# Performance work log

Hardware: AMD Instinct MI355X
Metric: run time of the kernel (lower is better)

Reference implementation:

```python
import jax, jax.numpy as jnp
import numpy as np
import math

B, S = 1, 2048
HID = 4096
NH = 32            # total query heads
NKV = 8            # total kv heads
D = HID // NH      # 128 head_dim
WIN = 1024         # sliding window (layer_idx=1 is odd and < num_layers//2)
LAYER = 1
THETA = 10000.0
LAMBDA_INIT = 0.8 - 0.6 * math.exp(-0.3 * LAYER)
SCALE = D ** -0.5
EPS = 1e-5
OP = NH * D + 2 * NKV * D  # Wqkv output size


def setup_inputs() -> dict:
    key = jax.random.key(0)
    ks = jax.random.split(key, 9)
    std = 0.02
    return {
        "hidden_states": jax.random.normal(ks[0], (B * S, HID), jnp.float32),
        "positions": jnp.tile(jnp.arange(S, dtype=jnp.int32), B),
        "Wqkv_w": jax.random.normal(ks[1], (OP, HID), jnp.float32) * std,
        "Wqkv_b": jnp.zeros((OP,), jnp.float32),
        "out_w": jax.random.normal(ks[2], (HID, NH * D), jnp.float32) * std,
        "out_b": jnp.zeros((HID,), jnp.float32),
        "lambda_q1": jax.random.normal(ks[3], (D,), jnp.float32) * 0.1,
        "lambda_k1": jax.random.normal(ks[4], (D,), jnp.float32) * 0.1,
        "lambda_q2": jax.random.normal(ks[5], (D,), jnp.float32) * 0.1,
        "lambda_k2": jax.random.normal(ks[6], (D,), jnp.float32) * 0.1,
        "subln_w": jnp.ones((2 * D,), jnp.float32),
    }


def _rope(x, pos):
    # neox-style rotary; x: [N, H, D], pos: [N]
    half = D // 2
    inv_freq = 1.0 / (THETA ** (jnp.arange(half, dtype=jnp.float32) / half))
    ang = pos.astype(jnp.float32)[:, None] * inv_freq[None, :]      # [N, half]
    cos = jnp.cos(ang)[:, None, :]
    sin = jnp.sin(ang)[:, None, :]
    x1, x2 = x[..., :half], x[..., half:]
    return jnp.concatenate([x1 * cos - x2 * sin, x2 * cos + x1 * sin], axis=-1)


def _probs(q, k, mask):
    # q: [B,S,Hq,D], k: [B,S,Hkv,D] -> softmax probs [B,Hq,S,S] with GQA repeat
    g = q.shape[2] // k.shape[2]
    k = jnp.repeat(k, g, axis=2)
    scores = jnp.einsum('bqhd,bkhd->bhqk', q, k) * SCALE
    scores = jnp.where(mask, scores, -1e30)
    return jax.nn.softmax(scores, axis=-1)


def _pv(p, v, g):
    # p: [B,Hq,S,S], v: [B,S,Hkv,D]
    v = jnp.repeat(v, g, axis=2)
    return jnp.einsum('bhqk,bkhd->bqhd', p, v)


def reference(hidden_states, positions, Wqkv_w, Wqkv_b, out_w, out_b,
              lambda_q1, lambda_k1, lambda_q2, lambda_k2, subln_w):
    qkv = hidden_states @ Wqkv_w.T + Wqkv_b                 # [N, OP]
    q, k, v = jnp.split(qkv, [NH * D, NH * D + NKV * D], axis=-1)
    q = q.reshape(-1, NH, D)
    k = k.reshape(-1, NKV, D)
    v = v.reshape(-1, NKV, D)
    q = _rope(q, positions)
    k = _rope(k, positions)

    q = q.reshape(B, S, NH, D)
    k = k.reshape(B, S, NKV, D)
    v = v.reshape(B, S, NKV, D)
    # split_heads: '(H two) D' -> even heads = group1, odd heads = group2
    q1, q2 = q[:, :, 0::2], q[:, :, 1::2]
    k1, k2 = k[:, :, 0::2], k[:, :, 1::2]
    v1, v2 = v[:, :, 0::2], v[:, :, 1::2]

    i = jnp.arange(S)[:, None]
    j = jnp.arange(S)[None, :]
    mask = (j <= i) & ((i - j) < WIN)                        # causal + sliding window

    g = (NH // 2) // (NKV // 2)
    p1 = _probs(q1, k1, mask)
    p2 = _probs(q2, k2, mask)
    a11 = _pv(p1, v1, g)
    a12 = _pv(p1, v2, g)
    a21 = _pv(p2, v1, g)
    a22 = _pv(p2, v2, g)

    attn1 = jnp.concatenate([a11, a12], axis=-1)             # [B,S,NH/2,2D]
    attn2 = jnp.concatenate([a21, a22], axis=-1)

    lam = (jnp.exp(jnp.sum(lambda_q1 * lambda_k1))
           - jnp.exp(jnp.sum(lambda_q2 * lambda_k2)) + LAMBDA_INIT)
    attn = attn1 - lam * attn2

    # subln: RMSNorm over last dim (2*head_dim)
    var = jnp.mean(attn * attn, axis=-1, keepdims=True)
    attn = attn * jax.lax.rsqrt(var + EPS) * subln_w
    attn = attn * (1.0 - LAMBDA_INIT)

    attn = attn.reshape(B * S, NH * D)
    return attn @ out_w.T + out_b
```

## Files before the change

kernel.cpp:

```cpp
#include <hip/hip_runtime.h>

typedef unsigned short u16;
typedef __attribute__((ext_vector_type(8))) short bf16x8;
typedef __attribute__((ext_vector_type(4))) float f32x4;
typedef __attribute__((ext_vector_type(4))) unsigned short us4;
typedef __attribute__((ext_vector_type(8))) unsigned short us8;

#define S_LEN 2048
#define QKV_P 6144
#define WIN_SZ 1024
#define SCALE_F 0.08838834764831845f
#define LAMBDA_INIT_F 0.35550906759096925f
#define ONE_MINUS_LI_F 0.6444909324090308f

__device__ __forceinline__ u16 f2bf(float f) {
    union { float f; unsigned int u; } v; v.f = f;
    unsigned int u = v.u;
    return (u16)((u + 0x7fffu + ((u >> 16) & 1u)) >> 16);
}
__device__ __forceinline__ float bf2f(u16 u) {
    union { unsigned int u; float f; } v; v.u = ((unsigned int)u) << 16; return v.f;
}
__device__ __forceinline__ void gload16(const void* g, void* l) {
    __builtin_amdgcn_global_load_lds(
        (const __attribute__((address_space(1))) unsigned int*)g,
        (__attribute__((address_space(3))) unsigned int*)l, 16, 0, 0);
}

__global__ __launch_bounds__(256)
void conv_f32_bf16(const float* __restrict__ src, u16* __restrict__ dst, int n4) {
    for (int i = blockIdx.x * 256 + threadIdx.x; i < n4; i += gridDim.x * 256) {
        float4 v = ((const float4*)src)[i];
        us4 h;
        h.x = f2bf(v.x); h.y = f2bf(v.y); h.z = f2bf(v.z); h.w = f2bf(v.w);
        ((us4*)dst)[i] = h;
    }
}

template<int NR>
__device__ __forceinline__ void stage_half(const u16* __restrict__ src, int K,
                                           int gRowBase, int kcol0,
                                           u16* slot, int tid, int wid) {
#pragma unroll
    for (int g = 0; g < (NR + 127) / 128; ++g) {
        if (g * 128 + wid * 16 < NR) {
            int row = g * 128 + (tid >> 2);
            int cc = (tid & 3) ^ ((row >> 1) & 3);
            gload16(src + (size_t)(gRowBase + row) * K + kcol0 + cc * 8,
                    slot + g * 4096 + wid * 512);
        }
    }
}

__device__ __forceinline__ bf16x8 ldfrag(const u16* slot, int row, int l4) {
    int pc = l4 ^ ((row >> 1) & 3);
    return *(const bf16x8*)(slot + row * 32 + pc * 8);
}

template<int BM, int NF>
__device__ __forceinline__ void gemm_wait(int wid) {
    if constexpr (BM == 256 && NF == 3) {
        if (wid < 4) asm volatile("s_waitcnt vmcnt(4)" ::: "memory");
        else         asm volatile("s_waitcnt vmcnt(3)" ::: "memory");
    } else if constexpr (BM == 128 && NF == 4) {
        asm volatile("s_waitcnt vmcnt(3)" ::: "memory");
    } else {
        asm volatile("s_waitcnt vmcnt(0)" ::: "memory");
    }
}

template<int BM, int NF, int OUT_BF16>
__global__ __launch_bounds__(512)
__attribute__((amdgpu_waves_per_eu(2, 2)))
void gemm8p(const u16* __restrict__ A, const u16* __restrict__ W,
            const float* __restrict__ bias, void* __restrict__ Cv,
            int M, int N, int K) {
    constexpr int BN = NF * 64;
    constexpr int ASLOT = BM * 32;
    constexpr int BSLOT = NF * 2048;
    constexpr int MFRAG = BM / 32;
    __shared__ u16 lds[4 * ASLOT + 4 * BSLOT];

    const int tid = threadIdx.x;
    const int wid = tid >> 6, lane = tid & 63;
    const int wr = wid >> 2, wc = wid & 3;
    const int l15 = lane & 15, l4 = lane >> 4;

    int by, bx;
    {
        const int x = blockIdx.x & 7, j = blockIdx.x >> 3;
        if (BM == 256) { by = (x >> 2) * 4 + (j >> 3); bx = (x & 3) * 8 + (j & 7); }
        else           { by = (x >> 2) * 8 + (j & 7);  bx = (x & 3) * 4 + (j >> 3); }
    }
    const int rowBase = by * BM;
    const int colBase = bx * BN;

    const int NT = K >> 6;

    u16* const baseA = lds;
    u16* const baseB = lds + 4 * ASLOT;

    f32x4 acc[MFRAG][NF] = {};

    stage_half<BM>(A, K, rowBase, 0,  baseA + 0 * ASLOT, tid, wid);
    stage_half<BN>(W, K, colBase, 0,  baseB + 0 * BSLOT, tid, wid);
    stage_half<BM>(A, K, rowBase, 32, baseA + 1 * ASLOT, tid, wid);
    stage_half<BN>(W, K, colBase, 32, baseB + 1 * BSLOT, tid, wid);
    stage_half<BM>(A, K, rowBase, 64, baseA + 2 * ASLOT, tid, wid);
    stage_half<BN>(W, K, colBase, 64, baseB + 2 * BSLOT, tid, wid);
    gemm_wait<BM, NF>(wid);
    __builtin_amdgcn_s_barrier();

    for (int t = 0; t < NT; ++t) {
        const int b = t & 1;
        const int bn = b ^ 1;
        u16* const A0 = baseA + (b * 2 + 0) * ASLOT;
        u16* const A1 = baseA + (b * 2 + 1) * ASLOT;
        u16* const B0 = baseB + (b * 2 + 0) * BSLOT;
        u16* const B1 = baseB + (b * 2 + 1) * BSLOT;

        bf16x8 af[MFRAG], bfv[NF];

#pragma unroll
        for (int m = 0; m < MFRAG; ++m) af[m] = ldfrag(A0, wr * (BM / 2) + m * 16 + l15, l4);
#pragma unroll
        for (int n = 0; n < NF; ++n) bfv[n] = ldfrag(B0, wc * (NF * 16) + n * 16 + l15, l4);
        if (t + 1 < NT) {
            stage_half<BM>(A, K, rowBase, (t + 1) * 64 + 32, baseA + (bn * 2 + 1) * ASLOT, tid, wid);
            stage_half<BN>(W, K, colBase, (t + 1) * 64 + 32, baseB + (bn * 2 + 1) * BSLOT, tid, wid);
        }
        __builtin_amdgcn_s_barrier();
        __builtin_amdgcn_s_setprio(1);
#pragma unroll
        for (int m = 0; m < MFRAG; ++m)
#pragma unroll
            for (int n = 0; n < NF; ++n)
                acc[m][n] = __builtin_amdgcn_mfma_f32_16x16x32_bf16(af[m], bfv[n], acc[m][n], 0, 0, 0);
        __builtin_amdgcn_s_setprio(0);
        __builtin_amdgcn_s_barrier();

#pragma unroll
        for (int m = 0; m < MFRAG; ++m) af[m] = ldfrag(A1, wr * (BM / 2) + m * 16 + l15, l4);
#pragma unroll
        for (int n = 0; n < NF; ++n) bfv[n] = ldfrag(B1, wc * (NF * 16) + n * 16 + l15, l4);
        if (t + 2 < NT) {
            stage_half<BM>(A, K, rowBase, (t + 2) * 64, baseA + (b * 2 + 0) * ASLOT, tid, wid);
            stage_half<BN>(W, K, colBase, (t + 2) * 64, baseB + (b * 2 + 0) * BSLOT, tid, wid);
        }
        __builtin_amdgcn_s_barrier();
        __builtin_amdgcn_s_setprio(1);
#pragma unroll
        for (int m = 0; m < MFRAG; ++m)
#pragma unroll
            for (int n = 0; n < NF; ++n)
                acc[m][n] = __builtin_amdgcn_mfma_f32_16x16x32_bf16(af[m], bfv[n], acc[m][n], 0, 0, 0);
        __builtin_amdgcn_s_setprio(0);
        if (t + 2 < NT) gemm_wait<BM, NF>(wid);
        else            asm volatile("s_waitcnt vmcnt(0)" ::: "memory");
        __builtin_amdgcn_s_barrier();
    }

#pragma unroll
    for (int n = 0; n < NF; ++n) {
        int col = colBase + wc * (NF * 16) + n * 16 + l15;
        float bs = bias[col];
#pragma unroll
        for (int m = 0; m < MFRAG; ++m)
#pragma unroll
            for (int rr = 0; rr < 4; ++rr) {
                int rowi = rowBase + wr * (BM / 2) + m * 16 + l4 * 4 + rr;
                float v = acc[m][n][rr] + bs;
                if (OUT_BF16) ((u16*)Cv)[(size_t)rowi * N + col] = f2bf(v);
                else          ((float*)Cv)[(size_t)rowi * N + col] = v;
            }
    }
}

__global__ __launch_bounds__(256)
void rope_bf16(u16* __restrict__ qkv, const int* __restrict__ positions) {
    const int row = blockIdx.x;
    const float pos = (float)positions[row];
    for (int idx = threadIdx.x; idx < 640; idx += 256) {
        int head = idx >> 4;
        int g = idx & 15;
        int base = (head < 32) ? head * 128 : 4096 + (head - 32) * 128;
        u16* p = qkv + (size_t)row * QKV_P + base + g * 4;
        us4 x1 = *(us4*)p;
        us4 x2 = *(us4*)(p + 64);
#pragma unroll
        for (int j = 0; j < 4; ++j) {
            float inv_freq = __expf(-(float)(g * 4 + j) * (9.210340371976184f / 64.0f));
            float ang = pos * inv_freq;
            float s, c;
            sincosf(ang, &s, &c);
            float a = bf2f(x1[j]), b = bf2f(x2[j]);
            x1[j] = f2bf(a * c - b * s);
            x2[j] = f2bf(b * c + a * s);
        }
        *(us4*)p = x1;
        *(us4*)(p + 64) = x2;
    }
}

__global__ __launch_bounds__(256)
void vtrans(const u16* __restrict__ qkv, u16* __restrict__ vt) {
    __shared__ u16 T[128 * 72];
    const int s0 = blockIdx.x * 64;
    const int a = blockIdx.y;
    const u16* src = qkv + 5120 + a * 128;
#pragma unroll
    for (int it = 0; it < 4; ++it) {
        int idx = it * 256 + threadIdx.x;
        int s = idx >> 4;
        int c8 = idx & 15;
        us8 v = *(const us8*)(src + (size_t)(s0 + s) * QKV_P + c8 * 8);
        int sc = s >> 3, su = s & 7;
#pragma unroll
        for (int j = 0; j < 8; ++j) {
            int d = c8 * 8 + j;
            T[d * 72 + ((sc ^ ((d >> 3) & 7)) * 8 + su)] = v[j];
        }
    }
    __syncthreads();
#pragma unroll
    for (int it = 0; it < 4; ++it) {
        int idx = it * 256 + threadIdx.x;
        int d = idx >> 3, sc = idx & 7;
        us8 v = *(const us8*)&T[d * 72 + ((sc ^ ((d >> 3) & 7)) * 8)];
        *(us8*)(vt + (size_t)a * 262144 + (size_t)d * 2048 + s0 + sc * 8) = v;
    }
}

__global__ __launch_bounds__(512)
__attribute__((amdgpu_waves_per_eu(2, 2)))
void attn_bf16(const u16* __restrict__ qkv, const u16* __restrict__ vtg,
               u16* __restrict__ attnb,
               const float* __restrict__ lq1, const float* __restrict__ lk1,
               const float* __restrict__ lq2, const float* __restrict__ lk2,
               const float* __restrict__ subln) {
    __shared__ u16 smem[73728];
#define KBUF(b, st) (smem + ((b) * 2 + (st)) * 8192)
#define VBUF(b, st) (smem + 32768 + ((b) * 2 + (st)) * 8192)

    const int tid = threadIdx.x;
    const int w = tid >> 6, lane = tid & 63;
    const int g = w & 3, sid = w >> 2;
    const int l15 = lane & 15, l4 = lane >> 4;
    u16* const Pw = smem + 65536 + w * 1024;

    int qb, h;
    {
        int i = blockIdx.x;
        if (i < 256) { qb = 16 + (i & 15); h = i >> 4; }
        else         { int j = i - 256; qb = j & 15; h = j >> 4; }
    }
    const int q0 = qb * 64;
    const int a1 = 2 * (h >> 2), a2 = a1 + 1;

    bf16x8 qf[4];
    {
        int qrow = q0 + g * 16 + l15;
        const u16* qp = qkv + (size_t)qrow * QKV_P + (2 * h + sid) * 128;
#pragma unroll
        for (int kk = 0; kk < 4; ++kk)
            qf[kk] = *(const bf16x8*)(qp + kk * 32 + l4 * 8);
    }

    bf16x8 onesf;
#pragma unroll
    for (int j = 0; j < 8; ++j) onesf[j] = (short)0x3F80;

    f32x4 aV1[8] = {}, aV2[8] = {};
    f32x4 l_acc = {};
    float m[4];
#pragma unroll
    for (int r = 0; r < 4; ++r) m[r] = -1e30f;

    const int kr4 = lane >> 4, kc = lane & 15;
    const int vd8 = lane >> 3, vc = lane & 7;

    const int tbeg = (qb >= 16) ? (qb - 16) : 0;
    const int tend = qb;

#define STAGE_TILE(T, NB)                                                      \
    {                                                                          \
        const int kv0s = (T) * 64;                                             \
        _Pragma("unroll")                                                      \
        for (int s2 = 0; s2 < 2; ++s2) {                                       \
            int ch = w * 2 + s2;                                               \
            int krow = ch * 4 + kr4;                                           \
            int kcs = (kc ^ (krow & 7)) * 8;                                   \
            const u16* kbase = qkv + (size_t)(kv0s + krow) * QKV_P + 4096;     \
            gload16(kbase + a1 * 128 + kcs, KBUF(NB, 0) + ch * 512);           \
            gload16(kbase + a2 * 128 + kcs, KBUF(NB, 1) + ch * 512);           \
            int vdrow = ch * 8 + vd8;                                          \
            int vcs = (vc ^ (vdrow & 7)) * 8;                                  \
            const u16* vbase = vtg + (size_t)vdrow * 2048 + kv0s + vcs;        \
            gload16(vbase + (size_t)a1 * 262144, VBUF(NB, 0) + ch * 512);      \
            gload16(vbase + (size_t)a2 * 262144, VBUF(NB, 1) + ch * 512);      \
        }                                                                      \
    }

    STAGE_TILE(tbeg, 0);
    asm volatile("s_waitcnt vmcnt(0)" ::: "memory");
    __builtin_amdgcn_s_barrier();
    asm volatile("" ::: "memory");

    int cb = 0;
    for (int t = tbeg; t <= tend; ++t) {
        const int kv0 = t * 64;

        if (t < tend) STAGE_TILE(t + 1, cb ^ 1);

        f32x4 sc[4];
        const u16* Kc = KBUF(cb, sid);
        __builtin_amdgcn_s_setprio(1);
#pragma unroll
        for (int c = 0; c < 4; ++c) {
            f32x4 s1 = {0.f, 0.f, 0.f, 0.f};
#pragma unroll
            for (int kk = 0; kk < 4; ++kk) {
                int off = (c * 16 + l15) * 128 + (((kk * 4 + l4) ^ (l15 & 7)) * 8);
                s1 = __builtin_amdgcn_mfma_f32_16x16x32_bf16(qf[kk], *(const bf16x8*)&Kc[off], s1, 0, 0, 0);
            }
            sc[c] = s1;
        }
        __builtin_amdgcn_s_setprio(0);

        const bool dz = (t == tend);
        const bool wz = (qb >= 16) && (t <= tbeg + 1);
        if (dz) {
#pragma unroll
            for (int c = 0; c < 4; ++c) {
                int j = kv0 + c * 16 + l15;
#pragma unroll
                for (int r = 0; r < 4; ++r) {
                    int i = q0 + g * 16 + l4 * 4 + r;
                    if (j > i) sc[c][r] = -1e30f;
                }
            }
        } else if (wz) {
#pragma unroll
            for (int c = 0; c < 4; ++c) {
                int j = kv0 + c * 16 + l15;
#pragma unroll
                for (int r = 0; r < 4; ++r) {
                    int i = q0 + g * 16 + l4 * 4 + r;
                    if (i - j >= WIN_SZ) sc[c][r] = -1e30f;
                }
            }
        }

        float lmax[4];
#pragma unroll
        for (int r = 0; r < 4; ++r)
            lmax[r] = fmaxf(fmaxf(sc[0][r], sc[1][r]), fmaxf(sc[2][r], sc[3][r]));
        bool need = false;
#pragma unroll
        for (int r = 0; r < 4; ++r)
            need = need || (lmax[r] > m[r] + 32.0f);
        if (__any(need)) {
            float rmax[4];
#pragma unroll
            for (int r = 0; r < 4; ++r) rmax[r] = lmax[r];
#pragma unroll
            for (int msk = 1; msk < 16; msk <<= 1)
#pragma unroll
                for (int r = 0; r < 4; ++r)
                    rmax[r] = fmaxf(rmax[r], __shfl_xor(rmax[r], msk));
            float fr[4];
#pragma unroll
            for (int r = 0; r < 4; ++r) {
                float nm = fmaxf(m[r], rmax[r]);
                fr[r] = __expf((m[r] - nm) * SCALE_F);
                m[r] = nm;
                l_acc[r] *= fr[r];
            }
#pragma unroll
            for (int f = 0; f < 8; ++f)
#pragma unroll
                for (int r = 0; r < 4; ++r) {
                    aV1[f][r] *= fr[r];
                    aV2[f][r] *= fr[r];
                }
        }

#pragma unroll
        for (int c = 0; c < 4; ++c) {
            int col = c * 16 + l15;
#pragma unroll
            for (int r = 0; r < 4; ++r) {
                int prow = l4 * 4 + r;
                float p = __expf((sc[c][r] - m[r]) * SCALE_F);
                if (wz && (m[r] < -1e29f)) p = 0.f;
                int pco = ((col >> 3) ^ (prow & 7)) * 8 + (col & 7);
                Pw[prow * 64 + pco] = f2bf(p);
            }
        }

        const u16* V0 = VBUF(cb, 0);
        const u16* V1 = VBUF(cb, 1);
        __builtin_amdgcn_s_setprio(1);
#pragma unroll
        for (int kk = 0; kk < 2; ++kk) {
            int pch = ((kk * 4 + l4) ^ (l15 & 7)) * 8;
            bf16x8 pa = *(const bf16x8*)&Pw[l15 * 64 + pch];
            l_acc = __builtin_amdgcn_mfma_f32_16x16x32_bf16(pa, onesf, l_acc, 0, 0, 0);
#pragma unroll
            for (int f = 0; f < 8; ++f) {
                int off = (f * 16 + l15) * 64 + (((kk * 4 + l4) ^ (l15 & 7)) * 8);
                aV1[f] = __builtin_amdgcn_mfma_f32_16x16x32_bf16(pa, *(const bf16x8*)&V0[off], aV1[f], 0, 0, 0);
                aV2[f] = __builtin_amdgcn_mfma_f32_16x16x32_bf16(pa, *(const bf16x8*)&V1[off], aV2[f], 0, 0, 0);
            }
        }
        __builtin_amdgcn_s_setprio(0);

        asm volatile("s_waitcnt vmcnt(0)" ::: "memory");
        __builtin_amdgcn_s_barrier();
        asm volatile("" ::: "memory");
        cb ^= 1;
    }

    float s1v = lq1[lane] * lk1[lane] + lq1[lane + 64] * lk1[lane + 64];
    float s2v = lq2[lane] * lk2[lane] + lq2[lane + 64] * lk2[lane + 64];
#pragma unroll
    for (int msk = 1; msk < 64; msk <<= 1) {
        s1v += __shfl_xor(s1v, msk);
        s2v += __shfl_xor(s2v, msk);
    }
    const float lam = __expf(s1v) - __expf(s2v) + LAMBDA_INIT_F;

    float* const Cmb = (float*)smem;
    if (sid == 1) {
#pragma unroll
        for (int r = 0; r < 4; ++r) {
            float inv2 = lam / l_acc[r];
            int row = g * 16 + l4 * 4 + r;
#pragma unroll
            for (int f = 0; f < 8; ++f) {
                Cmb[row * 264 + f * 16 + l15]       = aV1[f][r] * inv2;
                Cmb[row * 264 + 128 + f * 16 + l15] = aV2[f][r] * inv2;
            }
        }
    }
    __syncthreads();
    if (sid == 0) {
        float sw0[8], sw1[8];
#pragma unroll
        for (int f = 0; f < 8; ++f) {
            sw0[f] = subln[f * 16 + l15];
            sw1[f] = subln[128 + f * 16 + l15];
        }
#pragma unroll
        for (int r = 0; r < 4; ++r) {
            float inv1 = 1.0f / l_acc[r];
            int row = g * 16 + l4 * 4 + r;
            float o0[8], o1[8];
            float ssq = 0.f;
#pragma unroll
            for (int f = 0; f < 8; ++f) {
                o0[f] = aV1[f][r] * inv1 - Cmb[row * 264 + f * 16 + l15];
                o1[f] = aV2[f][r] * inv1 - Cmb[row * 264 + 128 + f * 16 + l15];
                ssq += o0[f] * o0[f] + o1[f] * o1[f];
            }
#pragma unroll
            for (int msk = 1; msk < 16; msk <<= 1) ssq += __shfl_xor(ssq, msk);
            float scale = rsqrtf(ssq * (1.0f / 256.0f) + 1e-5f) * ONE_MINUS_LI_F;
            u16* op = attnb + (size_t)(q0 + row) * 4096 + h * 256;
#pragma unroll
            for (int f = 0; f < 8; ++f) {
                op[f * 16 + l15]       = f2bf(o0[f] * scale * sw0[f]);
                op[128 + f * 16 + l15] = f2bf(o1[f] * scale * sw1[f]);
            }
        }
    }
#undef STAGE_TILE
#undef KBUF
#undef VBUF
}

extern "C" void kernel_launch(void* const* d_in, const int* in_sizes, int n_in,
                              void* d_out, int out_size, void* d_ws, size_t ws_size,
                              hipStream_t stream) {
    const float* hidden    = (const float*)d_in[0];
    const int*   positions = (const int*)d_in[1];
    const float* Wqkv_w    = (const float*)d_in[2];
    const float* Wqkv_b    = (const float*)d_in[3];
    const float* out_w     = (const float*)d_in[4];
    const float* out_b     = (const float*)d_in[5];
    const float* lq1       = (const float*)d_in[6];
    const float* lk1       = (const float*)d_in[7];
    const float* lq2       = (const float*)d_in[8];
    const float* lk2       = (const float*)d_in[9];
    const float* subln     = (const float*)d_in[10];
    float* out = (float*)d_out;

    u16* ws0   = (u16*)d_ws;
    u16* hb    = ws0;
    u16* wqb   = ws0 + 8388608;
    u16* qkvb  = ws0 + 33554432;
    u16* attnb = ws0;
    u16* owb   = ws0 + 8388608;
    u16* vt    = ws0 + 25165824;

    conv_f32_bf16<<<2048, 256, 0, stream>>>(hidden, hb, 2048 * 4096 / 4);
    conv_f32_bf16<<<2048, 256, 0, stream>>>(Wqkv_w, wqb, 6144 * 4096 / 4);

    gemm8p<256, 3, 1><<<256, 512, 0, stream>>>(hb, wqb, Wqkv_b, qkvb, 2048, 6144, 4096);

    rope_bf16<<<S_LEN, 256, 0, stream>>>(qkvb, positions);
    vtrans<<<dim3(32, 8), 256, 0, stream>>>(qkvb, vt);

    conv_f32_bf16<<<2048, 256, 0, stream>>>(out_w, owb, 4096 * 4096 / 4);

    attn_bf16<<<512, 512, 0, stream>>>(qkvb, vt, attnb, lq1, lk1, lq2, lk2, subln);

    gemm8p<128, 4, 0><<<256, 512, 0, stream>>>(attnb, owb, out_b, out, 2048, 4096, 4096);
}
```

Baseline: 337.7 us.

## Deepen GEMM prefetch pipelines and drop redundant barriers in QKV and output GEMMs

The QKV GEMM drops the barrier between issuing the next half-tile loads and the MFMA phase, and waits with a deeper vmcnt so two half-tiles stay in flight. The output projection GEMM gets its own kernel with a three-buffer ring of full 64-wide K tiles, prefetching two tiles ahead with one barrier per iteration. The aim is to hide global-to-LDS latency and cut synchronisation overhead. The cost is more LDS for the output GEMM, and the vmcnt accounting must be exactly right to avoid races.

```diff
diff --git a/kernel.cpp b/kernel.cpp
--- a/kernel.cpp
+++ b/kernel.cpp
@@ -57,25 +57,21 @@
     return *(const bf16x8*)(slot + row * 32 + pc * 8);
 }
 
-template<int BM, int NF>
-__device__ __forceinline__ void gemm_wait(int wid) {
-    if constexpr (BM == 256 && NF == 3) {
-        if (wid < 4) asm volatile("s_waitcnt vmcnt(4)" ::: "memory");
-        else         asm volatile("s_waitcnt vmcnt(3)" ::: "memory");
-    } else if constexpr (BM == 128 && NF == 4) {
-        asm volatile("s_waitcnt vmcnt(3)" ::: "memory");
-    } else {
-        asm volatile("s_waitcnt vmcnt(0)" ::: "memory");
-    }
-}
-
-template<int BM, int NF, int OUT_BF16>
+__device__ __forceinline__ void qkv_wait_deep(int wid) {
+    if (wid < 4) asm volatile("s_waitcnt vmcnt(8)" ::: "memory");
+    else         asm volatile("s_waitcnt vmcnt(6)" ::: "memory");
+}
+__device__ __forceinline__ void qkv_wait_half(int wid) {
+    if (wid < 4) asm volatile("s_waitcnt vmcnt(4)" ::: "memory");
+    else         asm volatile("s_waitcnt vmcnt(3)" ::: "memory");
+}
+
 __global__ __launch_bounds__(512)
 __attribute__((amdgpu_waves_per_eu(2, 2)))
-void gemm8p(const u16* __restrict__ A, const u16* __restrict__ W,
-            const float* __restrict__ bias, void* __restrict__ Cv,
-            int M, int N, int K) {
-    constexpr int BN = NF * 64;
+void gemm_qkv(const u16* __restrict__ A, const u16* __restrict__ W,
+              const float* __restrict__ bias, u16* __restrict__ C,
+              int M, int N, int K) {
+    constexpr int BM = 256, NF = 3, BN = NF * 64;
     constexpr int ASLOT = BM * 32;
     constexpr int BSLOT = NF * 2048;
     constexpr int MFRAG = BM / 32;
@@ -86,12 +82,9 @@
     const int wr = wid >> 2, wc = wid & 3;
     const int l15 = lane & 15, l4 = lane >> 4;
 
-    int by, bx;
-    {
-        const int x = blockIdx.x & 7, j = blockIdx.x >> 3;
-        if (BM == 256) { by = (x >> 2) * 4 + (j >> 3); bx = (x & 3) * 8 + (j & 7); }
-        else           { by = (x >> 2) * 8 + (j & 7);  bx = (x & 3) * 4 + (j >> 3); }
-    }
+    const int x = blockIdx.x & 7, j = blockIdx.x >> 3;
+    const int by = (x >> 2) * 4 + (j >> 3);
+    const int bx = (x & 3) * 8 + (j & 7);
     const int rowBase = by * BM;
     const int colBase = bx * BN;
 
@@ -108,7 +101,7 @@
     stage_half<BN>(W, K, colBase, 32, baseB + 1 * BSLOT, tid, wid);
     stage_half<BM>(A, K, rowBase, 64, baseA + 2 * ASLOT, tid, wid);
     stage_half<BN>(W, K, colBase, 64, baseB + 2 * BSLOT, tid, wid);
-    gemm_wait<BM, NF>(wid);
+    qkv_wait_half(wid);
     __builtin_amdgcn_s_barrier();
 
     for (int t = 0; t < NT; ++t) {
@@ -129,7 +122,6 @@
             stage_half<BM>(A, K, rowBase, (t + 1) * 64 + 32, baseA + (bn * 2 + 1) * ASLOT, tid, wid);
             stage_half<BN>(W, K, colBase, (t + 1) * 64 + 32, baseB + (bn * 2 + 1) * BSLOT, tid, wid);
         }
-        __builtin_amdgcn_s_barrier();
         __builtin_amdgcn_s_setprio(1);
 #pragma unroll
         for (int m = 0; m < MFRAG; ++m)
@@ -137,6 +129,8 @@
             for (int n = 0; n < NF; ++n)
                 acc[m][n] = __builtin_amdgcn_mfma_f32_16x16x32_bf16(af[m], bfv[n], acc[m][n], 0, 0, 0);
         __builtin_amdgcn_s_setprio(0);
+        if (t == NT - 1) asm volatile("s_waitcnt vmcnt(0)" ::: "memory");
+        else             qkv_wait_deep(wid);
         __builtin_amdgcn_s_barrier();
 
 #pragma unroll
@@ -147,7 +141,6 @@
             stage_half<BM>(A, K, rowBase, (t + 2) * 64, baseA + (b * 2 + 0) * ASLOT, tid, wid);
             stage_half<BN>(W, K, colBase, (t + 2) * 64, baseB + (b * 2 + 0) * BSLOT, tid, wid);
         }
-        __builtin_amdgcn_s_barrier();
         __builtin_amdgcn_s_setprio(1);
 #pragma unroll
         for (int m = 0; m < MFRAG; ++m)
@@ -155,8 +148,9 @@
             for (int n = 0; n < NF; ++n)
                 acc[m][n] = __builtin_amdgcn_mfma_f32_16x16x32_bf16(af[m], bfv[n], acc[m][n], 0, 0, 0);
         __builtin_amdgcn_s_setprio(0);
-        if (t + 2 < NT) gemm_wait<BM, NF>(wid);
-        else            asm volatile("s_waitcnt vmcnt(0)" ::: "memory");
+        if (t <= NT - 3)      qkv_wait_deep(wid);
+        else if (t == NT - 2) qkv_wait_half(wid);
+        else                  asm volatile("s_waitcnt vmcnt(0)" ::: "memory");
         __builtin_amdgcn_s_barrier();
     }
 
@@ -169,9 +163,93 @@
 #pragma unroll
             for (int rr = 0; rr < 4; ++rr) {
                 int rowi = rowBase + wr * (BM / 2) + m * 16 + l4 * 4 + rr;
-                float v = acc[m][n][rr] + bs;
-                if (OUT_BF16) ((u16*)Cv)[(size_t)rowi * N + col] = f2bf(v);
-                else          ((float*)Cv)[(size_t)rowi * N + col] = v;
+                C[(size_t)rowi * N + col] = f2bf(acc[m][n][rr] + bs);
+            }
+    }
+}
+
+__global__ __launch_bounds__(512)
+__attribute__((amdgpu_waves_per_eu(2, 2)))
+void gemm_out(const u16* __restrict__ A, const u16* __restrict__ W,
+              const float* __restrict__ bias, float* __restrict__ C,
+              int M, int N, int K) {
+    constexpr int BM = 128, BN = 256;
+    constexpr int AT = BM * 64;
+    constexpr int BT = BN * 64;
+    __shared__ u16 lds[3 * (AT + BT)];
+
+    const int tid = threadIdx.x;
+    const int wid = tid >> 6, lane = tid & 63;
+    const int wr = wid >> 2, wc = wid & 3;
+    const int l15 = lane & 15, l4 = lane >> 4;
+
+    const int x = blockIdx.x & 7, j = blockIdx.x >> 3;
+    const int by = (x >> 2) * 8 + (j & 7);
+    const int bx = (x & 3) * 4 + (j >> 3);
+    const int rowBase = by * BM, colBase = bx * BN;
+    const int NT = K >> 6;
+
+    u16* const baseA = lds;
+    u16* const baseB = lds + 3 * AT;
+
+    f32x4 acc[4][4] = {};
+
+#define STAGE3(T, nb)                                                          \
+    {                                                                          \
+        stage_half<BM>(A, K, rowBase, (T) * 64,      baseA + (nb) * AT, tid, wid);           \
+        stage_half<BM>(A, K, rowBase, (T) * 64 + 32, baseA + (nb) * AT + BM * 32, tid, wid); \
+        stage_half<BN>(W, K, colBase, (T) * 64,      baseB + (nb) * BT, tid, wid);           \
+        stage_half<BN>(W, K, colBase, (T) * 64 + 32, baseB + (nb) * BT + BN * 32, tid, wid); \
+    }
+
+    STAGE3(0, 0);
+    STAGE3(1, 1);
+    asm volatile("s_waitcnt vmcnt(6)" ::: "memory");
+    __builtin_amdgcn_s_barrier();
+
+    int cur = 0;
+    for (int t = 0; t < NT; ++t) {
+        u16* const Ab = baseA + cur * AT;
+        u16* const Bb = baseB + cur * BT;
+
+        bf16x8 a0[4], a1[4], b0[4], b1[4];
+#pragma unroll
+        for (int m2 = 0; m2 < 4; ++m2) {
+            a0[m2] = ldfrag(Ab,           wr * 64 + m2 * 16 + l15, l4);
+            a1[m2] = ldfrag(Ab + BM * 32, wr * 64 + m2 * 16 + l15, l4);
+            b0[m2] = ldfrag(Bb,           wc * 64 + m2 * 16 + l15, l4);
+            b1[m2] = ldfrag(Bb + BN * 32, wc * 64 + m2 * 16 + l15, l4);
+        }
+        if (t + 2 < NT) {
+            int nb = cur + 2; if (nb >= 3) nb -= 3;
+            STAGE3(t + 2, nb);
+        }
+        __builtin_amdgcn_s_setprio(1);
+#pragma unroll
+        for (int m2 = 0; m2 < 4; ++m2)
+#pragma unroll
+            for (int n = 0; n < 4; ++n) {
+                acc[m2][n] = __builtin_amdgcn_mfma_f32_16x16x32_bf16(a0[m2], b0[n], acc[m2][n], 0, 0, 0);
+                acc[m2][n] = __builtin_amdgcn_mfma_f32_16x16x32_bf16(a1[m2], b1[n], acc[m2][n], 0, 0, 0);
+            }
+        __builtin_amdgcn_s_setprio(0);
+        if (t <= NT - 3)      asm volatile("s_waitcnt vmcnt(6)" ::: "memory");
+        else if (t == NT - 2) asm volatile("s_waitcnt vmcnt(0)" ::: "memory");
+        __builtin_amdgcn_s_barrier();
+        cur = cur + 1; if (cur == 3) cur = 0;
+    }
+#undef STAGE3
+
+#pragma unroll
+    for (int n = 0; n < 4; ++n) {
+        int col = colBase + wc * 64 + n * 16 + l15;
+        float bs = bias[col];
+#pragma unroll
+        for (int m2 = 0; m2 < 4; ++m2)
+#pragma unroll
+            for (int rr = 0; rr < 4; ++rr) {
+                int rowi = rowBase + wr * 64 + m2 * 16 + l4 * 4 + rr;
+                C[(size_t)rowi * N + col] = acc[m2][n][rr] + bs;
             }
     }
 }
@@ -506,7 +584,7 @@
     conv_f32_bf16<<<2048, 256, 0, stream>>>(hidden, hb, 2048 * 4096 / 4);
     conv_f32_bf16<<<2048, 256, 0, stream>>>(Wqkv_w, wqb, 6144 * 4096 / 4);
 
-    gemm8p<256, 3, 1><<<256, 512, 0, stream>>>(hb, wqb, Wqkv_b, qkvb, 2048, 6144, 4096);
+    gemm_qkv<<<256, 512, 0, stream>>>(hb, wqb, Wqkv_b, qkvb, 2048, 6144, 4096);
 
     rope_bf16<<<S_LEN, 256, 0, stream>>>(qkvb, positions);
     vtrans<<<dim3(32, 8), 256, 0, stream>>>(qkvb, vt);
@@ -515,5 +593,5 @@
 
     attn_bf16<<<512, 512, 0, stream>>>(qkvb, vt, attnb, lq1, lk1, lq2, lk2, subln);
 
-    gemm8p<128, 4, 0><<<256, 512, 0, stream>>>(attnb, owb, out_b, out, 2048, 4096, 4096);
-}
+    gemm_out<<<256, 512, 0, stream>>>(attnb, owb, out_b, out, 2048, 4096, 4096);
+}
```

Measured after the change: 331.6 us (median of 2 runs). Within noise of the previous version (-1.8%).
